# Optimization experiments

Hardware: AMD Instinct MI355X
Metric: run time of the kernel (lower is better)

## Reference

```python
import jax, jax.numpy as jnp
import numpy as np


def _apply1(state, w, m00, m01, m10, m11):
    # state: (N,16) complex64; apply 2x2 gate on wire w (wire 0 = most significant bit)
    st = state.reshape(-1, 2 ** w, 2, 2 ** (3 - w))
    a, b = st[:, :, 0, :], st[:, :, 1, :]
    def bc(v):
        return jnp.reshape(jnp.asarray(v, state.dtype), (-1, 1, 1))
    na = bc(m00) * a + bc(m01) * b
    nb = bc(m10) * a + bc(m11) * b
    return jnp.stack([na, nb], axis=2).reshape(-1, 16)


def _ry(state, theta, w):
    c, s = jnp.cos(theta / 2), jnp.sin(theta / 2)
    return _apply1(state, w, c, -s, s, c)


def _rx(state, theta, w):
    c, s = jnp.cos(theta / 2), jnp.sin(theta / 2)
    return _apply1(state, w, c, -1j * s, -1j * s, c)


def _rz(state, theta, w):
    e = jnp.exp(-0.5j * theta.astype(jnp.complex64))
    return _apply1(state, w, e, 0.0, 0.0, jnp.conj(e))


def _cnot(state, ctrl, tgt):
    s = state.reshape((-1, 2, 2, 2, 2))
    c_ax, t_ax = ctrl + 1, tgt + 1
    s0 = jnp.take(s, 0, axis=c_ax)
    s1 = jnp.take(s, 1, axis=c_ax)
    t2 = t_ax - (1 if t_ax > c_ax else 0)
    s1 = jnp.flip(s1, axis=t2)
    return jnp.stack([s0, s1], axis=c_ax).reshape(-1, 16)


def _measure_z(state):
    # expval of PauliZ on each wire: (N,4)
    p = (state.real ** 2 + state.imag ** 2).reshape(-1, 2, 2, 2, 2)
    z = jnp.array([1.0, -1.0], p.dtype)
    exps = []
    for w in range(4):
        axes = tuple(a for a in (1, 2, 3, 4) if a != w + 1)
        exps.append(p.sum(axes) @ z)
    return jnp.stack(exps, axis=1)


def setup_inputs() -> dict:
    key = jax.random.key(0)
    k = jax.random.split(key, 6)
    B = 2048
    x = jax.random.uniform(k[0], (B, 1, 28, 28), dtype=jnp.float32)
    emb_W = jax.random.normal(k[1], (4, 4), dtype=jnp.float32) * 0.5
    emb_b = jnp.zeros((4,), jnp.float32)
    q_params = jax.random.uniform(k[2], (5,), dtype=jnp.float32, minval=0.0, maxval=2.0 * np.pi)
    lin_W = jax.random.normal(k[3], (10, 784), dtype=jnp.float32) * (1.0 / np.sqrt(784.0))
    lin_b = jnp.zeros((10,), jnp.float32)
    return {"x": x, "emb_W": emb_W, "emb_b": emb_b, "q_params": q_params, "lin_W": lin_W, "lin_b": lin_b}


def reference(x, emb_W, emb_b, q_params, lin_W, lin_b):
    B = x.shape[0]
    img = x.reshape(B, 28, 28)
    # 2x2 non-overlapping patches, row-major over (r, c), ordered [tl, tr, bl, br]
    patches = img.reshape(B, 14, 2, 14, 2).transpose(0, 1, 3, 2, 4).reshape(B, 196, 4)
    ang = (patches @ emb_W.T + emb_b).reshape(-1, 4)  # (B*196, 4)
    N = ang.shape[0]
    state = jnp.zeros((N, 16), jnp.complex64).at[:, 0].set(1.0)
    # data encoding: RY(angle_i) on wire i
    for w in range(4):
        state = _ry(state, ang[:, w], w)
    # fixed 8-op random layer (learnable scalar rotation params + CNOT entanglers)
    state = _rx(state, q_params[0], 0)
    state = _ry(state, q_params[1], 1)
    state = _rz(state, q_params[2], 2)
    state = _cnot(state, 0, 1)
    state = _rx(state, q_params[3], 3)
    state = _cnot(state, 2, 3)
    state = _ry(state, q_params[4], 2)
    state = _cnot(state, 1, 2)
    feats = _measure_z(state).reshape(B, 196 * 4)  # patch-major concat, 4 expvals each
    logits = feats @ lin_W.T + lin_b
    return jax.nn.log_softmax(logits, axis=-1)
```

## Files before the change

### kernel.cpp

```cpp
#include <hip/hip_runtime.h>
#include <hip/hip_bf16.h>


template<int STRIDE>
__device__ __forceinline__ void ry_gate(float re[16], float im[16], float c, float s) {
    #pragma unroll
    for (int base = 0; base < 16; base += 2 * STRIDE) {
        #pragma unroll
        for (int off = 0; off < STRIDE; ++off) {
            const int i0 = base + off, i1 = i0 + STRIDE;
            const float r0 = re[i0], m0 = im[i0], r1 = re[i1], m1 = im[i1];
            re[i0] = c * r0 - s * r1;  im[i0] = c * m0 - s * m1;
            re[i1] = s * r0 + c * r1;  im[i1] = s * m0 + c * m1;
        }
    }
}

template<int STRIDE>
__device__ __forceinline__ void rx_gate(float re[16], float im[16], float c, float s) {
    #pragma unroll
    for (int base = 0; base < 16; base += 2 * STRIDE) {
        #pragma unroll
        for (int off = 0; off < STRIDE; ++off) {
            const int i0 = base + off, i1 = i0 + STRIDE;
            const float r0 = re[i0], m0 = im[i0], r1 = re[i1], m1 = im[i1];
            re[i0] = c * r0 + s * m1;  im[i0] = c * m0 - s * r1;
            re[i1] = s * m0 + c * r1;  im[i1] = -s * r0 + c * m1;
        }
    }
}

template<int STRIDE>
__device__ __forceinline__ void rz_gate(float re[16], float im[16], float c, float s) {
    #pragma unroll
    for (int base = 0; base < 16; base += 2 * STRIDE) {
        #pragma unroll
        for (int off = 0; off < STRIDE; ++off) {
            const int i0 = base + off, i1 = i0 + STRIDE;
            const float r0 = re[i0], m0 = im[i0], r1 = re[i1], m1 = im[i1];
            re[i0] = c * r0 + s * m0;  im[i0] = c * m0 - s * r0;
            re[i1] = c * r1 - s * m1;  im[i1] = s * r1 + c * m1;
        }
    }
}

template<int CMASK, int TMASK>
__device__ __forceinline__ void cnot_gate(float re[16], float im[16]) {
    #pragma unroll
    for (int i = 0; i < 16; ++i) {
        if ((i & CMASK) && !(i & TMASK)) {
            const int j = i | TMASK;
            float t;
            t = re[i]; re[i] = re[j]; re[j] = t;
            t = im[i]; im[i] = im[j]; im[j] = t;
        }
    }
}

__global__ __launch_bounds__(256) void quanv_fused(
    const float* __restrict__ x,
    const float* __restrict__ embW,
    const float* __restrict__ embB,
    const float* __restrict__ qp,
    const float* __restrict__ linW,
    const float* __restrict__ linB,
    float* __restrict__ out)
{
    const int b   = blockIdx.x;
    const int tid = threadIdx.x;

    __shared__ float sred[4][10];

    float part[10];
    #pragma unroll
    for (int c = 0; c < 10; ++c) part[c] = 0.0f;

    if (tid < 196) {
        const unsigned pi = (unsigned)tid / 14u, pj = (unsigned)tid % 14u;
        const float* img = x + (size_t)b * 784;
        const float2 r0 = *reinterpret_cast<const float2*>(img + (2 * pi) * 28 + 2 * pj);
        const float2 r1 = *reinterpret_cast<const float2*>(img + (2 * pi + 1) * 28 + 2 * pj);
        const float p0 = r0.x, p1 = r0.y, p2 = r1.x, p3 = r1.y;

        float cA[4], sA[4];
        #pragma unroll
        for (int w = 0; w < 4; ++w) {
            const float a = embB[w] + embW[4 * w + 0] * p0 + embW[4 * w + 1] * p1
                                    + embW[4 * w + 2] * p2 + embW[4 * w + 3] * p3;
            __sincosf(0.5f * a, &sA[w], &cA[w]);
        }

        float qc[5], qs[5];
        #pragma unroll
        for (int i = 0; i < 5; ++i) __sincosf(0.5f * qp[i], &qs[i], &qc[i]);

        float re[16], im[16];
        float ab[4], abc[8];
        ab[0] = cA[0] * cA[1];  ab[1] = cA[0] * sA[1];
        ab[2] = sA[0] * cA[1];  ab[3] = sA[0] * sA[1];
        #pragma unroll
        for (int j = 0; j < 4; ++j) {
            abc[2 * j]     = ab[j] * cA[2];
            abc[2 * j + 1] = ab[j] * sA[2];
        }
        #pragma unroll
        for (int k = 0; k < 8; ++k) {
            re[2 * k]     = abc[k] * cA[3];
            re[2 * k + 1] = abc[k] * sA[3];
            im[2 * k] = 0.0f;  im[2 * k + 1] = 0.0f;
        }

        rx_gate<8>(re, im, qc[0], qs[0]);
        ry_gate<4>(re, im, qc[1], qs[1]);
        rz_gate<2>(re, im, qc[2], qs[2]);
        cnot_gate<8, 4>(re, im);
        rx_gate<1>(re, im, qc[3], qs[3]);
        cnot_gate<2, 1>(re, im);
        ry_gate<2>(re, im, qc[4], qs[4]);
        cnot_gate<4, 2>(re, im);

        float p[16];
        #pragma unroll
        for (int i = 0; i < 16; ++i) p[i] = re[i] * re[i] + im[i] * im[i];

        float a8[8], a4[4], a2[2];
        float f0 = 0.0f, f1 = 0.0f, f2 = 0.0f;
        #pragma unroll
        for (int j = 0; j < 8; ++j) { a8[j] = p[j] + p[j + 8]; f0 += p[j] - p[j + 8]; }
        #pragma unroll
        for (int j = 0; j < 4; ++j) { a4[j] = a8[j] + a8[j + 4]; f1 += a8[j] - a8[j + 4]; }
        #pragma unroll
        for (int j = 0; j < 2; ++j) { a2[j] = a4[j] + a4[j + 2]; f2 += a4[j] - a4[j + 2]; }
        const float f3 = a2[0] - a2[1];

        #pragma unroll
        for (int c = 0; c < 10; ++c) {
            const float4 wv = *reinterpret_cast<const float4*>(linW + c * 784 + tid * 4);
            part[c] = f0 * wv.x + f1 * wv.y + f2 * wv.z + f3 * wv.w;
        }
    }

    #pragma unroll
    for (int c = 0; c < 10; ++c) {
        part[c] += __shfl_down(part[c], 32);
        part[c] += __shfl_down(part[c], 16);
        part[c] += __shfl_down(part[c], 8);
        part[c] += __shfl_down(part[c], 4);
        part[c] += __shfl_down(part[c], 2);
        part[c] += __shfl_down(part[c], 1);
    }
    const int lane = tid & 63;
    const int wv   = tid >> 6;
    if (lane == 0) {
        #pragma unroll
        for (int c = 0; c < 10; ++c) sred[wv][c] = part[c];
    }
    __syncthreads();

    if (tid < 16) {
        float logit = -1e30f;
        if (tid < 10)
            logit = sred[0][tid] + sred[1][tid] + sred[2][tid] + sred[3][tid] + linB[tid];
        float m = logit;
        m = fmaxf(m, __shfl_xor(m, 1, 16));
        m = fmaxf(m, __shfl_xor(m, 2, 16));
        m = fmaxf(m, __shfl_xor(m, 4, 16));
        m = fmaxf(m, __shfl_xor(m, 8, 16));
        float e = (tid < 10) ? expf(logit - m) : 0.0f;
        e += __shfl_xor(e, 1, 16);
        e += __shfl_xor(e, 2, 16);
        e += __shfl_xor(e, 4, 16);
        e += __shfl_xor(e, 8, 16);
        const float lse = m + logf(e);
        if (tid < 10) out[(size_t)b * 10 + tid] = logit - lse;
    }
}

extern "C" void kernel_launch(void* const* d_in, const int* in_sizes, int n_in,
                              void* d_out, int out_size, void* d_ws, size_t ws_size,
                              hipStream_t stream) {
    const float* x    = (const float*)d_in[0];
    const float* embW = (const float*)d_in[1];
    const float* embB = (const float*)d_in[2];
    const float* qp   = (const float*)d_in[3];
    const float* linW = (const float*)d_in[4];
    const float* linB = (const float*)d_in[5];
    float* out = (float*)d_out;

    const int B = in_sizes[0] / 784;
    quanv_fused<<<B, 256, 0, stream>>>(x, embW, embB, qp, linW, linB, out);
}
```

Baseline: 74.82 us.

## Stage features in shared memory and split linear layer across class-parallel threads

Instead of every patch thread computing all 10 class partial sums and doing 60 wavefront shuffle reductions, features are written to shared memory and 160 threads (16 per class) compute the dot products, reducing with 4 shuffles each. The first RX gate is also specialised for the purely real initial state, skipping the zero imaginary arithmetic. This adds a barrier and a strided loop with serial accumulation per thread, and the linW loads become less coalesced across classes.

```diff
diff --git a/kernel.cpp b/kernel.cpp
--- a/kernel.cpp
+++ b/kernel.cpp
@@ -69,11 +69,8 @@
     const int b   = blockIdx.x;
     const int tid = threadIdx.x;
 
-    __shared__ float sred[4][10];
-
-    float part[10];
-    #pragma unroll
-    for (int c = 0; c < 10; ++c) part[c] = 0.0f;
+    __shared__ float4 sfeats[196];
+    __shared__ float  slog[10];
 
     if (tid < 196) {
         const unsigned pi = (unsigned)tid / 14u, pj = (unsigned)tid % 14u;
@@ -107,10 +104,19 @@
         for (int k = 0; k < 8; ++k) {
             re[2 * k]     = abc[k] * cA[3];
             re[2 * k + 1] = abc[k] * sA[3];
-            im[2 * k] = 0.0f;  im[2 * k + 1] = 0.0f;
         }
 
-        rx_gate<8>(re, im, qc[0], qs[0]);
+        {
+            const float c = qc[0], s = qs[0];
+            #pragma unroll
+            for (int i0 = 0; i0 < 8; ++i0) {
+                const int i1 = i0 + 8;
+                const float r0 = re[i0], r1 = re[i1];
+                re[i0] = c * r0;   im[i0] = -s * r1;
+                re[i1] = c * r1;   im[i1] = -s * r0;
+            }
+        }
+
         ry_gate<4>(re, im, qc[1], qs[1]);
         rz_gate<2>(re, im, qc[2], qs[2]);
         cnot_gate<8, 4>(re, im);
@@ -133,34 +139,29 @@
         for (int j = 0; j < 2; ++j) { a2[j] = a4[j] + a4[j + 2]; f2 += a4[j] - a4[j + 2]; }
         const float f3 = a2[0] - a2[1];
 
-        #pragma unroll
-        for (int c = 0; c < 10; ++c) {
-            const float4 wv = *reinterpret_cast<const float4*>(linW + c * 784 + tid * 4);
-            part[c] = f0 * wv.x + f1 * wv.y + f2 * wv.z + f3 * wv.w;
+        sfeats[tid] = make_float4(f0, f1, f2, f3);
+    }
+    __syncthreads();
+
+    if (tid < 160) {
+        const int c = tid >> 4;
+        const int j = tid & 15;
+        float acc = 0.0f;
+        for (int p = j; p < 196; p += 16) {
+            const float4 f  = sfeats[p];
+            const float4 wv = *reinterpret_cast<const float4*>(linW + c * 784 + p * 4);
+            acc += f.x * wv.x + f.y * wv.y + f.z * wv.z + f.w * wv.w;
         }
-    }
-
-    #pragma unroll
-    for (int c = 0; c < 10; ++c) {
-        part[c] += __shfl_down(part[c], 32);
-        part[c] += __shfl_down(part[c], 16);
-        part[c] += __shfl_down(part[c], 8);
-        part[c] += __shfl_down(part[c], 4);
-        part[c] += __shfl_down(part[c], 2);
-        part[c] += __shfl_down(part[c], 1);
-    }
-    const int lane = tid & 63;
-    const int wv   = tid >> 6;
-    if (lane == 0) {
-        #pragma unroll
-        for (int c = 0; c < 10; ++c) sred[wv][c] = part[c];
+        acc += __shfl_xor(acc, 8);
+        acc += __shfl_xor(acc, 4);
+        acc += __shfl_xor(acc, 2);
+        acc += __shfl_xor(acc, 1);
+        if (j == 0) slog[c] = acc;
     }
     __syncthreads();
 
     if (tid < 16) {
-        float logit = -1e30f;
-        if (tid < 10)
-            logit = sred[0][tid] + sred[1][tid] + sred[2][tid] + sred[3][tid] + linB[tid];
+        const float logit = (tid < 10) ? (slog[tid] + linB[tid]) : -1e30f;
         float m = logit;
         m = fmaxf(m, __shfl_xor(m, 1, 16));
         m = fmaxf(m, __shfl_xor(m, 2, 16));
```

Result: no change. 74.70 us (-0.2%).
